# Kernel optimization log

Hardware: AMD Instinct MI355X
Metric: run time of the kernel (lower is better)

Reference implementation:

```python
import jax, jax.numpy as jnp
import numpy as np
from jax import lax

EPS = 1e-5
KV_DOWN = 4

def _bn(z, g, b, m, v):
    # eval-mode BatchNorm2d over channel axis 1
    inv = (g / jnp.sqrt(v + EPS))[None, :, None, None]
    return z * inv + (b - m * g / jnp.sqrt(v + EPS))[None, :, None, None]

def setup_inputs() -> dict:
    key = jax.random.key(0)
    ks = jax.random.split(key, 8)
    B, C, H, W = 8, 256, 128, 128
    AC, VC = 64, 128
    return {
        "x": jax.random.normal(ks[0], (B, C, H, W), jnp.float32),
        "wq": jax.random.normal(ks[1], (AC, C), jnp.float32) * 0.05,
        "wk": jax.random.normal(ks[2], (AC, C), jnp.float32) * 0.05,
        "wv": jax.random.normal(ks[3], (VC, C), jnp.float32) * 0.05,
        "wproj": jax.random.normal(ks[4], (C, VC), jnp.float32) * 0.05,
        "bn_g": jnp.ones((C,), jnp.float32),
        "bn_b": jnp.zeros((C,), jnp.float32),
        "bn_m": jax.random.normal(ks[5], (C,), jnp.float32) * 0.1,
        "bn_v": jax.random.uniform(ks[5], (C,), jnp.float32, 0.5, 1.5),
        "dw_w": jax.random.normal(ks[6], (C, 1, 3, 3), jnp.float32) * 0.1,
        "pw_w": jax.random.normal(ks[7], (C, C), jnp.float32) * 0.05,
        "mbn_g": jnp.ones((C,), jnp.float32),
        "mbn_b": jnp.zeros((C,), jnp.float32),
        "mbn_m": jax.random.normal(ks[7], (C,), jnp.float32) * 0.1,
        "mbn_v": jax.random.uniform(ks[6], (C,), jnp.float32, 0.5, 1.5),
    }

def reference(x, wq, wk, wv, wproj, bn_g, bn_b, bn_m, bn_v, dw_w, pw_w, mbn_g, mbn_b, mbn_m, mbn_v):
    b, c, h, w = x.shape
    d = KV_DOWN
    scale = wq.shape[0] ** -0.5
    # Q from full-res x via 1x1 conv
    q = jnp.einsum('ac,bchw->bahw', wq, x)            # [B,AC,H,W]
    # avg-pool x for K,V
    x_kv = x.reshape(b, c, h // d, d, w // d, d).mean(axis=(3, 5))
    k = jnp.einsum('ac,bchw->bahw', wk, x_kv)          # [B,AC,H',W']
    v = jnp.einsum('vc,bchw->bvhw', wv, x_kv)          # [B,VC,H',W']
    N = h * w
    M = (h // d) * (w // d)
    qf = q.reshape(b, -1, N)                           # [B,AC,N]
    kf = k.reshape(b, -1, M)                           # [B,AC,M]
    vf = v.reshape(b, -1, M)                           # [B,VC,M]
    attn = jnp.einsum('ban,bam->bnm', qf, kf) * scale  # [B,N,M]
    attn = jax.nn.softmax(attn, axis=-1)
    y = jnp.einsum('bnm,bvm->bvn', attn, vf)           # [B,VC,N]
    y = y.reshape(b, vf.shape[1], h, w)
    y = jnp.einsum('cv,bvhw->bchw', wproj, y)          # proj -> [B,C,H,W]
    y = jax.nn.silu(_bn(y, bn_g, bn_b, bn_m, bn_v))
    # depthwise 3x3 + pointwise 1x1 mix
    z = lax.conv_general_dilated(y, dw_w, (1, 1), 'SAME',
                                 dimension_numbers=('NCHW', 'OIHW', 'NCHW'),
                                 feature_group_count=c)
    z = jnp.einsum('oc,bchw->bohw', pw_w, z)
    z = _bn(z, mbn_g, mbn_b, mbn_m, mbn_v)
    return x + jax.nn.silu(z)
```

## Files before the change

### kernel.cpp

```cpp
#include <hip/hip_runtime.h>
#include <hip/hip_bf16.h>
#include <math.h>

#define EPSV 1e-5f

typedef short bf16x8 __attribute__((ext_vector_type(8)));
typedef float f32x16 __attribute__((ext_vector_type(16)));
typedef unsigned int uint4v __attribute__((ext_vector_type(4)));

__device__ __forceinline__ float silu_f(float v) { return v / (1.0f + __expf(-v)); }

__device__ __forceinline__ unsigned short f2bf(float f) {
  __hip_bfloat16 h = __float2bfloat16(f);
  return __builtin_bit_cast(unsigned short, h);
}

__device__ __forceinline__ float fexp2(float x) {
  float r;
  asm("v_exp_f32 %0, %1" : "=v"(r) : "v"(x));
  return r;
}

__device__ __forceinline__ unsigned int cvtpk(float lo, float hi) {
  unsigned int r;
  asm("v_cvt_pk_bf16_f32 %0, %1, %2" : "=v"(r) : "v"(lo), "v"(hi));
  return r;
}

__device__ __forceinline__ bf16x8 ld_frag(const unsigned short* p) {
  return *reinterpret_cast<const bf16x8*>(p);
}

__device__ __forceinline__ void gload16(const unsigned short* g, unsigned short* l) {
  __builtin_amdgcn_global_load_lds((const __attribute__((address_space(1))) void*)g,
                                   (__attribute__((address_space(3))) void*)l, 16, 0, 0);
}

__global__ __launch_bounds__(256) void pool_kernel(const float* __restrict__ x,
                                                   float* __restrict__ xkv) {
  int idx = blockIdx.x * 256 + threadIdx.x;
  int m = idx & 1023, bc = idx >> 10;
  int hh = m >> 5, ww = m & 31;
  const float* base = x + ((size_t)bc << 14) + (size_t)(hh * 4) * 128 + ww * 4;
  float s = 0.f;
#pragma unroll
  for (int i = 0; i < 4; ++i) {
    float4 v = *reinterpret_cast<const float4*>(base + i * 128);
    s += v.x + v.y + v.z + v.w;
  }
  xkv[idx] = s * 0.0625f;
}

__global__ __launch_bounds__(256) void cvtT_kernel(const float* __restrict__ x,
                                                   unsigned short* __restrict__ xbfT) {
  __shared__ unsigned short sT[64 * 68];
  const int tid = threadIdx.x;
  const int b = blockIdx.z, c0 = blockIdx.y * 64, n0 = blockIdx.x * 64;
  const float* xs = x + ((size_t)(b * 256 + c0) << 14) + n0;
#pragma unroll
  for (int pass = 0; pass < 4; ++pass) {
    int cc = (tid >> 4) + pass * 16;
    int col = (tid & 15) * 4;
    float4 v = *reinterpret_cast<const float4*>(xs + ((size_t)cc << 14) + col);
    unsigned short* d = &sT[cc * 68 + col];
    d[0] = f2bf(v.x); d[1] = f2bf(v.y); d[2] = f2bf(v.z); d[3] = f2bf(v.w);
  }
  __syncthreads();
  int n = tid >> 2, cs = (tid & 3) * 16;
  unsigned short tmp[16];
#pragma unroll
  for (int i = 0; i < 16; ++i) tmp[i] = sT[(cs + i) * 68 + n];
  unsigned short* dst = xbfT + (((size_t)b * 16384 + n0 + n) << 8) + c0 + cs;
  *reinterpret_cast<uint4*>(dst) = *reinterpret_cast<uint4*>(tmp);
  *reinterpret_cast<uint4*>(dst + 8) = *reinterpret_cast<uint4*>(tmp + 8);
}

__global__ __launch_bounds__(256) void prep_all(const float* __restrict__ wproj,
                                                const float* __restrict__ bng,
                                                const float* __restrict__ bnb,
                                                const float* __restrict__ bnm,
                                                const float* __restrict__ bnv,
                                                const float* __restrict__ pww,
                                                const float* __restrict__ wq,
                                                unsigned short* __restrict__ wpb,
                                                float* __restrict__ bnsc,
                                                float* __restrict__ bnsh,
                                                unsigned short* __restrict__ pwPack,
                                                unsigned short* __restrict__ wqPack) {
  int i = blockIdx.x * 256 + threadIdx.x;
  if (i < 32768) {
    int j = i & 7, lane = (i >> 3) & 63, kc = (i >> 9) & 7, ctcg = i >> 12;
    int row = (ctcg >> 2) * 128 + (ctcg & 3) * 32 + (lane & 31);
    int col = kc * 16 + (lane >> 5) * 8 + j;
    wpb[i] = f2bf(wproj[row * 128 + col]);
  } else if (i < 33024) {
    int c = i - 32768;
    float inv = bng[c] / sqrtf(bnv[c] + EPSV);
    bnsc[c] = inv;
    bnsh[c] = bnb[c] - bnm[c] * inv;
  } else if (i < 98560) {
    int f = i - 33024;
    int j = f & 7, lane = (f >> 3) & 63, ks = (f >> 9) & 15, mt = f >> 13;
    int o = mt * 32 + (lane & 31);
    int cc = ks * 16 + (lane >> 5) * 8 + j;
    pwPack[f] = f2bf(pww[o * 256 + cc]);
  } else if (i < 114944) {
    int g = i - 98560;
    int j = g & 7, lane = (g >> 3) & 63, ks = (g >> 9) & 15, mt = g >> 13;
    int o = mt * 32 + (lane & 31);
    int cc = ks * 16 + (lane >> 5) * 8 + j;
    wqPack[g] = f2bf(wq[o * 256 + cc] * 0.18033688011112042f);
  }
}

__global__ __launch_bounds__(256, 4) void gemm_kv(const float* __restrict__ wk,
                                                  const float* __restrict__ wv,
                                                  const float* __restrict__ X,
                                                  unsigned short* __restrict__ Kt,
                                                  unsigned short* __restrict__ Vbf) {
  __shared__ float sW[64 * 68];
  __shared__ float sX[64 * 68];
  const int tid = threadIdx.x;
  const int n0 = blockIdx.x * 64;
  const int part = blockIdx.y;
  const int m0 = (part == 0) ? 0 : (part - 1) * 64;
  const float* W = (part == 0) ? wk : wv;
  const size_t xoff = (size_t)blockIdx.z * 256 * 1024;
  const int tm4 = (tid >> 4) * 4, tn4 = (tid & 15) * 4;
  float acc[4][4] = {};
  for (int k0 = 0; k0 < 256; k0 += 64) {
    __syncthreads();
#pragma unroll
    for (int i = 0; i < 16; ++i) {
      int flat = tid + i * 256;
      int kk = flat & 63, mm = flat >> 6;
      sW[kk * 68 + mm] = W[(m0 + mm) * 256 + k0 + kk];
      sX[kk * 68 + mm] = X[xoff + (size_t)(k0 + kk) * 1024 + n0 + mm];
    }
    __syncthreads();
#pragma unroll 8
    for (int k = 0; k < 64; ++k) {
      float4 a4 = *reinterpret_cast<const float4*>(&sW[k * 68 + tm4]);
      float4 b4 = *reinterpret_cast<const float4*>(&sX[k * 68 + tn4]);
      float av[4] = {a4.x, a4.y, a4.z, a4.w};
      float bv[4] = {b4.x, b4.y, b4.z, b4.w};
#pragma unroll
      for (int i = 0; i < 4; ++i)
#pragma unroll
        for (int j = 0; j < 4; ++j) acc[i][j] += av[i] * bv[j];
    }
  }
  if (part == 0) {
    const size_t coff = (size_t)blockIdx.z * 65536;
#pragma unroll
    for (int j = 0; j < 4; ++j) {
      ushort4 o;
      o.x = f2bf(acc[0][j]); o.y = f2bf(acc[1][j]);
      o.z = f2bf(acc[2][j]); o.w = f2bf(acc[3][j]);
      *reinterpret_cast<ushort4*>(&Kt[coff + (size_t)(n0 + tn4 + j) * 64 + tm4]) = o;
    }
  } else {
    const size_t coff = (size_t)blockIdx.z * 131072;
#pragma unroll
    for (int i = 0; i < 4; ++i) {
      ushort4 o;
      o.x = f2bf(acc[i][0]); o.y = f2bf(acc[i][1]);
      o.z = f2bf(acc[i][2]); o.w = f2bf(acc[i][3]);
      *reinterpret_cast<ushort4*>(&Vbf[coff + (size_t)(m0 + tm4 + i) * 1024 + n0 + tn4]) = o;
    }
  }
}

__global__ __launch_bounds__(256, 4) void qgemm_mfma(const unsigned short* __restrict__ xbfT,
                                                     const unsigned short* __restrict__ wqPack,
                                                     unsigned short* __restrict__ Qt) {
  __shared__ __align__(16) unsigned short sX[2][128 * 64];
  const int tid = threadIdx.x;
  const int w = tid >> 6, l = tid & 63;
  const int lq = l & 31, hi = l >> 5;
  const int b = blockIdx.y;
  const int n0 = blockIdx.x * 128;
  const int lr8 = l >> 3;
  const int gslot = (l & 7) ^ (lr8 & 7);
  const unsigned short* xb = xbfT + (((size_t)b * 16384 + n0) << 8);

#define QSTAGE(buf, ck)                                                       \
  {                                                                           \
    _Pragma("unroll") for (int i = 0; i < 4; ++i) {                           \
      int row = w * 32 + i * 8;                                               \
      gload16(xb + ((size_t)(row + lr8) << 8) + (ck) * 64 + gslot * 8,        \
              &sX[buf][row * 64]);                                            \
    }                                                                         \
  }

  f32x16 acc0, acc1;
#pragma unroll
  for (int i = 0; i < 16; ++i) { acc0[i] = 0.f; acc1[i] = 0.f; }

  QSTAGE(0, 0);
  __syncthreads();
  int cur = 0;
  for (int ck = 0; ck < 4; ++ck) {
    if (ck < 3) QSTAGE(cur ^ 1, ck + 1);
    const unsigned short* xl = sX[cur];
#pragma unroll
    for (int k2 = 0; k2 < 4; ++k2) {
      bf16x8 bfr = ld_frag(xl + (w * 32 + lq) * 64 + (((2 * k2 + hi) ^ (lq & 7)) << 3));
      int ks = ck * 4 + k2;
      bf16x8 a0 = ld_frag(wqPack + (size_t)((ks)*64 + l) * 8);
      bf16x8 a1 = ld_frag(wqPack + (size_t)((16 + ks) * 64 + l) * 8);
      acc0 = __builtin_amdgcn_mfma_f32_32x32x16_bf16(a0, bfr, acc0, 0, 0, 0);
      acc1 = __builtin_amdgcn_mfma_f32_32x32x16_bf16(a1, bfr, acc1, 0, 0, 0);
    }
    __syncthreads();
    cur ^= 1;
  }
#undef QSTAGE

  unsigned short* so2 = (unsigned short*)sX + w * 2304;
#pragma unroll
  for (int r = 0; r < 16; ++r) {
    int a = (r & 3) + 8 * (r >> 2) + 4 * hi;
    so2[lq * 72 + a] = f2bf(acc0[r]);
    so2[lq * 72 + 32 + a] = f2bf(acc1[r]);
  }
#pragma unroll
  for (int pass = 0; pass < 4; ++pass) {
    int flat = pass * 64 + l;
    int row = flat >> 3, col8 = (flat & 7) * 8;
    bf16x8 v = ld_frag(so2 + row * 72 + col8);
    *reinterpret_cast<bf16x8*>(Qt + ((size_t)b * 16384 + n0 + w * 32 + row) * 64 + col8) = v;
  }
}

__global__ __launch_bounds__(256, 3) void attn_mfma(
    const unsigned short* __restrict__ Qt, const unsigned short* __restrict__ Kt,
    const unsigned short* __restrict__ Vb, const unsigned short* __restrict__ wpb,
    const float* __restrict__ bnsc, const float* __restrict__ bnsh,
    unsigned short* __restrict__ yact) {
  __shared__ __align__(16) unsigned char smem[49152];
  unsigned short* const sK = (unsigned short*)smem;
  unsigned short* const sV = (unsigned short*)(smem + 16384);
  const int tid = threadIdx.x;
  const int w = tid >> 6, l = tid & 63;
  const int lq = l & 31, hi = l >> 5;
  const int bid = blockIdx.x;
  const int b = bid >> 7;
  const int q0 = (bid & 127) * 128 + w * 32;

  const unsigned short* Qp = Qt + ((size_t)b * 16384 + q0 + lq) * 64 + hi * 8;
  bf16x8 qf[4];
#pragma unroll
  for (int kc = 0; kc < 4; ++kc) qf[kc] = ld_frag(Qp + kc * 16);

  const uint4v ow = {0x3F803F80u, 0x3F803F80u, 0x3F803F80u, 0x3F803F80u};
  const bf16x8 onesf = __builtin_bit_cast(bf16x8, ow);

  f32x16 acc[4], accS;
#pragma unroll
  for (int t = 0; t < 4; ++t)
#pragma unroll
    for (int i = 0; i < 16; ++i) acc[t][i] = 0.f;
#pragma unroll
  for (int i = 0; i < 16; ++i) accS[i] = 0.f;

  const unsigned short* Kb = Kt + (size_t)b * 65536;
  const unsigned short* Vbb = Vb + (size_t)b * 131072;
  const int lr8 = l >> 3;
  const int gslot = (l & 7) ^ (lr8 & 7);

#define STAGE(buf, ch)                                                           \
  {                                                                              \
    const int m0s = (ch) * 64;                                                   \
    _Pragma("unroll") for (int i = 0; i < 2; ++i) {                              \
      int row8 = w * 16 + i * 8;                                                 \
      gload16(Kb + (size_t)(m0s + row8 + lr8) * 64 + gslot * 8,                  \
              sK + (buf) * 4096 + row8 * 64);                                    \
    }                                                                            \
    _Pragma("unroll") for (int j = 0; j < 4; ++j) {                              \
      int vc8 = w * 32 + j * 8;                                                  \
      gload16(Vbb + (size_t)(vc8 + lr8) * 1024 + m0s + gslot * 8,                \
              sV + (buf) * 8192 + vc8 * 64);                                     \
    }                                                                            \
  }

  STAGE(0, 0);
  __syncthreads();
  int cur = 0;
  for (int ch = 0; ch < 16; ++ch) {
    if (ch < 15) STAGE(cur ^ 1, ch + 1);
    const unsigned short* kb = sK + cur * 4096;
    const unsigned short* vb = sV + cur * 8192;
#pragma unroll
    for (int msi = 0; msi < 2; ++msi) {
      const int ms = msi * 32;
      bf16x8 kf[4];
#pragma unroll
      for (int kc = 0; kc < 4; ++kc)
        kf[kc] = ld_frag(kb + (ms + lq) * 64 + (((2 * kc + hi) ^ (lq & 7)) << 3));
      f32x16 sa;
#pragma unroll
      for (int i = 0; i < 16; ++i) sa[i] = 0.f;
      __builtin_amdgcn_s_setprio(1);
#pragma unroll
      for (int kc = 0; kc < 4; ++kc)
        sa = __builtin_amdgcn_mfma_f32_32x32x16_bf16(kf[kc], qf[kc], sa, 0, 0, 0);
      __builtin_amdgcn_s_setprio(0);

      float p[16];
#pragma unroll
      for (int r = 0; r < 16; ++r) p[r] = fexp2(sa[r] - 16.0f);

      unsigned int wpk[8];
#pragma unroll
      for (int i = 0; i < 8; ++i) wpk[i] = cvtpk(p[2 * i], p[2 * i + 1]);
      auto s01 = __builtin_amdgcn_permlane32_swap(wpk[0], wpk[2], false, false);
      auto s23 = __builtin_amdgcn_permlane32_swap(wpk[1], wpk[3], false, false);
      auto s45 = __builtin_amdgcn_permlane32_swap(wpk[4], wpk[6], false, false);
      auto s67 = __builtin_amdgcn_permlane32_swap(wpk[5], wpk[7], false, false);
      uint4v f0 = {(unsigned int)s01[0], (unsigned int)s23[0], (unsigned int)s01[1],
                   (unsigned int)s23[1]};
      uint4v f1 = {(unsigned int)s45[0], (unsigned int)s67[0], (unsigned int)s45[1],
                   (unsigned int)s67[1]};
      bf16x8 pf0 = __builtin_bit_cast(bf16x8, f0);
      bf16x8 pf1 = __builtin_bit_cast(bf16x8, f1);

      __builtin_amdgcn_s_setprio(1);
#pragma unroll
      for (int t = 0; t < 4; ++t) {
        bf16x8 vf0 =
            ld_frag(vb + (t * 32 + lq) * 64 + ((((ms >> 3) + hi) ^ (lq & 7)) << 3));
        bf16x8 vf1 =
            ld_frag(vb + (t * 32 + lq) * 64 + ((((ms >> 3) + 2 + hi) ^ (lq & 7)) << 3));
        acc[t] = __builtin_amdgcn_mfma_f32_32x32x16_bf16(pf0, vf0, acc[t], 0, 0, 0);
        acc[t] = __builtin_amdgcn_mfma_f32_32x32x16_bf16(pf1, vf1, acc[t], 0, 0, 0);
      }
      accS = __builtin_amdgcn_mfma_f32_32x32x16_bf16(pf0, onesf, accS, 0, 0, 0);
      accS = __builtin_amdgcn_mfma_f32_32x32x16_bf16(pf1, onesf, accS, 0, 0, 0);
      __builtin_amdgcn_s_setprio(0);
    }
    __syncthreads();
    cur ^= 1;
  }
#undef STAGE

  unsigned short* so = (unsigned short*)smem + w * 4096;
#pragma unroll
  for (int t = 0; t < 4; ++t)
#pragma unroll
    for (int r = 0; r < 16; ++r) {
      int q = (r & 3) + 8 * (r >> 2) + 4 * hi;
      int col = t * 32 + lq;
      so[q * 128 + (col ^ ((q & 15) << 3))] = f2bf(acc[t][r] / accS[r]);
    }
  __syncthreads();

  bf16x8 of[8];
#pragma unroll
  for (int kc = 0; kc < 8; ++kc) {
    int colr = kc * 16 + hi * 8;
    of[kc] = ld_frag(&so[lq * 128 + (colr ^ ((lq & 15) << 3))]);
  }
#pragma unroll
  for (int cg = 0; cg < 2; ++cg) {
    f32x16 z[4];
#pragma unroll
    for (int t = 0; t < 4; ++t)
#pragma unroll
      for (int i = 0; i < 16; ++i) z[t][i] = 0.f;
#pragma unroll
    for (int ct = 0; ct < 4; ++ct) {
      const unsigned short* wp = wpb + (size_t)(cg * 4 + ct) * 4096 + (size_t)l * 8;
#pragma unroll
      for (int kc = 0; kc < 8; ++kc) {
        bf16x8 wf = ld_frag(wp + kc * 512);
        z[ct] = __builtin_amdgcn_mfma_f32_32x32x16_bf16(wf, of[kc], z[ct], 0, 0, 0);
      }
    }
#pragma unroll
    for (int ct = 0; ct < 4; ++ct)
#pragma unroll
      for (int r = 0; r < 16; ++r) {
        int c = cg * 128 + ct * 32 + (r & 3) + 8 * (r >> 2) + 4 * hi;
        float val = z[ct][r] * bnsc[c] + bnsh[c];
        yact[((size_t)(b * 256 + c)) * 16384 + q0 + lq] = f2bf(silu_f(val));
      }
  }
}

__global__ __launch_bounds__(256, 4) void dwconv_kernel(const unsigned short* __restrict__ yact,
                                                        const float* __restrict__ dww,
                                                        unsigned short* __restrict__ D) {
  __shared__ unsigned int sP[130 * 67];
  const int tid = threadIdx.x;
  const int bc = blockIdx.x;
  const int c = bc & 255;
  for (int s = tid; s < 130 * 67; s += 256) sP[s] = 0;
  __syncthreads();
  const unsigned int* ysrc = reinterpret_cast<const unsigned int*>(yact) + (size_t)bc * 8192;
#pragma unroll
  for (int i = 0; i < 8; ++i) {
    int wi4 = tid + 256 * i;
    uint4 v = *reinterpret_cast<const uint4*>(ysrc + (size_t)wi4 * 4);
    int row = wi4 >> 4;
    int cw = (wi4 & 15) * 4;
    unsigned int* dst = &sP[(row + 1) * 67 + 1 + cw];
    dst[0] = v.x; dst[1] = v.y; dst[2] = v.z; dst[3] = v.w;
  }
  __syncthreads();
  float w9[9];
#pragma unroll
  for (int k = 0; k < 9; ++k) w9[k] = dww[c * 9 + k];
#pragma unroll
  for (int it = 0; it < 4; ++it) {
    int u = tid + 256 * it;
    int rho = u >> 4;
    int wg = u & 15;
    float a0[8] = {}, a1[8] = {};
#pragma unroll
    for (int ir = 0; ir < 4; ++ir) {
      int srow = rho * 2 + ir;
      const unsigned int* rp = &sP[srow * 67 + 4 * wg];
      float f[12];
#pragma unroll
      for (int k = 0; k < 6; ++k) {
        unsigned int wv = rp[k];
        f[2 * k] = __builtin_bit_cast(float, wv << 16);
        f[2 * k + 1] = __builtin_bit_cast(float, wv & 0xffff0000u);
      }
      if (ir < 3) {
#pragma unroll
        for (int cc = 0; cc < 8; ++cc)
#pragma unroll
          for (int dc = 0; dc < 3; ++dc) a0[cc] += f[cc + 1 + dc] * w9[ir * 3 + dc];
      }
      if (ir > 0) {
#pragma unroll
        for (int cc = 0; cc < 8; ++cc)
#pragma unroll
          for (int dc = 0; dc < 3; ++dc) a1[cc] += f[cc + 1 + dc] * w9[(ir - 1) * 3 + dc];
      }
    }
    uint4v o0, o1;
#pragma unroll
    for (int k = 0; k < 4; ++k) {
      o0[k] = (unsigned int)f2bf(a0[2 * k]) | ((unsigned int)f2bf(a0[2 * k + 1]) << 16);
      o1[k] = (unsigned int)f2bf(a1[2 * k]) | ((unsigned int)f2bf(a1[2 * k + 1]) << 16);
    }
    size_t ob = (size_t)bc * 8192 + (size_t)(rho * 2) * 64 + wg * 4;
    unsigned int* Dw = reinterpret_cast<unsigned int*>(D);
    *reinterpret_cast<uint4v*>(Dw + ob) = o0;
    *reinterpret_cast<uint4v*>(Dw + ob + 64) = o1;
  }
}

__global__ __launch_bounds__(256, 2) void pwmix_kernel(
    const unsigned short* __restrict__ D, const unsigned short* __restrict__ pwPack,
    const float* __restrict__ x, const float* __restrict__ mg,
    const float* __restrict__ mb2, const float* __restrict__ mmu,
    const float* __restrict__ mvv, float* __restrict__ out) {
  __shared__ unsigned int sDt[16384];
  __shared__ float smsc[256], smsh[256];
  const int tid = threadIdx.x;
  const int w = tid >> 6, l = tid & 63;
  const int lq = l & 31, hi = l >> 5;
  const int h = blockIdx.x, b = blockIdx.y;
  if (tid < 256) {
    float inv = mg[tid] * rsqrtf(mvv[tid] + EPSV);
    smsc[tid] = inv;
    smsh[tid] = mb2[tid] - mmu[tid] * inv;
  }
  const size_t dbase = ((size_t)b * 256) * 16384 + (size_t)h * 128;
#pragma unroll
  for (int i = 0; i < 8; ++i) {
    int cp = 64 * (i & 1) + 16 * w + (l >> 2);
    int pg = (l & 3) + 4 * (i >> 1);
    const unsigned short* g0 = D + dbase + (size_t)(cp * 2) * 16384 + pg * 8;
    bf16x8 d0 = ld_frag(g0);
    bf16x8 d1 = ld_frag(g0 + 16384);
#pragma unroll
    for (int j = 0; j < 8; ++j) {
      unsigned int word = ((unsigned int)(unsigned short)d0[j]) |
                          (((unsigned int)(unsigned short)d1[j]) << 16);
      int widx = ((pg * 8 + j) * 128 + cp) ^ (j << 2);
      sDt[widx] = word;
    }
  }
  __syncthreads();

  f32x16 z[2][4];
#pragma unroll
  for (int mti = 0; mti < 2; ++mti)
#pragma unroll
    for (int nt = 0; nt < 4; ++nt)
#pragma unroll
      for (int i = 0; i < 16; ++i) z[mti][nt][i] = 0.f;

#pragma unroll
  for (int ks = 0; ks < 16; ++ks) {
    bf16x8 a0 = ld_frag(pwPack + (size_t)(((w * 2 + 0) * 16 + ks) * 64 + l) * 8);
    bf16x8 a1 = ld_frag(pwPack + (size_t)(((w * 2 + 1) * 16 + ks) * 64 + l) * 8);
    bf16x8 bfr[4];
#pragma unroll
    for (int nt = 0; nt < 4; ++nt) {
      int word = ((nt * 32 + lq) * 128 + 8 * ks + 4 * hi) ^ ((lq & 7) << 2);
      bfr[nt] = *reinterpret_cast<const bf16x8*>(
          reinterpret_cast<const unsigned short*>(sDt) + (size_t)word * 2);
    }
#pragma unroll
    for (int nt = 0; nt < 4; ++nt) {
      z[0][nt] = __builtin_amdgcn_mfma_f32_32x32x16_bf16(a0, bfr[nt], z[0][nt], 0, 0, 0);
      z[1][nt] = __builtin_amdgcn_mfma_f32_32x32x16_bf16(a1, bfr[nt], z[1][nt], 0, 0, 0);
    }
  }

#pragma unroll
  for (int mti = 0; mti < 2; ++mti) {
    int ob = (w * 2 + mti) * 32 + 4 * hi;
#pragma unroll
    for (int r = 0; r < 16; ++r) {
      int o = ob + (r & 3) + 8 * (r >> 2);
      float sc = smsc[o], sh = smsh[o];
#pragma unroll
      for (int nt = 0; nt < 4; ++nt) {
        int px = nt * 32 + lq;
        size_t gi = (((size_t)(b * 256 + o)) << 14) + (size_t)h * 128 + px;
        float val = z[mti][nt][r] * sc + sh;
        out[gi] = x[gi] + silu_f(val);
      }
    }
  }
}

extern "C" void kernel_launch(void* const* d_in, const int* in_sizes, int n_in,
                              void* d_out, int out_size, void* d_ws, size_t ws_size,
                              hipStream_t stream) {
  const float* x     = (const float*)d_in[0];
  const float* wq    = (const float*)d_in[1];
  const float* wk    = (const float*)d_in[2];
  const float* wvp   = (const float*)d_in[3];
  const float* wproj = (const float*)d_in[4];
  const float* bng   = (const float*)d_in[5];
  const float* bnb   = (const float*)d_in[6];
  const float* bnm   = (const float*)d_in[7];
  const float* bnv   = (const float*)d_in[8];
  const float* dww   = (const float*)d_in[9];
  const float* pww   = (const float*)d_in[10];
  const float* mg    = (const float*)d_in[11];
  const float* mb2   = (const float*)d_in[12];
  const float* mmu   = (const float*)d_in[13];
  const float* mvv   = (const float*)d_in[14];
  float* out = (float*)d_out;

  char* base = (char*)d_ws;
  unsigned short* D = (unsigned short*)base;
  float* xkv = (float*)base;
  unsigned short* Qt  = (unsigned short*)(base + 8388608);
  unsigned short* Kt  = (unsigned short*)(base + 25165824);
  unsigned short* Vbf = (unsigned short*)(base + 26214400);
  unsigned short* wqPack = (unsigned short*)(base + 28311552);
  float* bnsc = (float*)(base + 67108864);
  float* bnsh = (float*)(base + 67109888);
  unsigned short* wpb    = (unsigned short*)(base + 67110912);
  unsigned short* pwPack = (unsigned short*)(base + 67176448);
  unsigned short* yact   = (unsigned short*)(base + 67307520);
  unsigned short* xbfT   = yact;

  cvtT_kernel<<<dim3(256, 4, 8), 256, 0, stream>>>(x, xbfT);
  pool_kernel<<<8192, 256, 0, stream>>>(x, xkv);
  prep_all<<<449, 256, 0, stream>>>(wproj, bng, bnb, bnm, bnv, pww, wq, wpb, bnsc, bnsh,
                                    pwPack, wqPack);
  gemm_kv<<<dim3(16, 3, 8), 256, 0, stream>>>(wk, wvp, xkv, Kt, Vbf);
  qgemm_mfma<<<dim3(128, 8), 256, 0, stream>>>(xbfT, wqPack, Qt);
  attn_mfma<<<dim3(1024), 256, 0, stream>>>(Qt, Kt, Vbf, wpb, bnsc, bnsh, yact);
  dwconv_kernel<<<2048, 256, 0, stream>>>(yact, dww, D);
  pwmix_kernel<<<dim3(128, 8), 256, 0, stream>>>(D, pwPack, x, mg, mb2, mmu, mvv, out);
}
```

Before: 282.5 us.

## Fuse depthwise 3x3 conv into pointwise mix kernel, dropping intermediate buffer

Merges the depthwise convolution and the pointwise mix into one kernel. Each block handles one image row: it loads a 3-row halo of the activation per 16-channel chunk into LDS, computes the depthwise output on the fly, and writes it as packed bf16 pairs directly into the transposed LDS tile that the MFMA pointwise GEMM consumes. This removes the write and read of the full intermediate D tensor plus one launch. In exchange each activation row is read three times from global memory (cached in L2), with 16 sync-separated chunk iterations and lower per-block parallelism for the depthwise work.

```diff
diff --git a/kernel.cpp b/kernel.cpp
--- a/kernel.cpp
+++ b/kernel.cpp
@@ -25,6 +25,13 @@
   unsigned int r;
   asm("v_cvt_pk_bf16_f32 %0, %1, %2" : "=v"(r) : "v"(lo), "v"(hi));
   return r;
+}
+
+__device__ __forceinline__ float bfu_lo(unsigned int w) {
+  return __builtin_bit_cast(float, w << 16);
+}
+__device__ __forceinline__ float bfu_hi(unsigned int w) {
+  return __builtin_bit_cast(float, w & 0xffff0000u);
 }
 
 __device__ __forceinline__ bf16x8 ld_frag(const unsigned short* p) {
@@ -388,78 +395,14 @@
   }
 }
 
-__global__ __launch_bounds__(256, 4) void dwconv_kernel(const unsigned short* __restrict__ yact,
-                                                        const float* __restrict__ dww,
-                                                        unsigned short* __restrict__ D) {
-  __shared__ unsigned int sP[130 * 67];
-  const int tid = threadIdx.x;
-  const int bc = blockIdx.x;
-  const int c = bc & 255;
-  for (int s = tid; s < 130 * 67; s += 256) sP[s] = 0;
-  __syncthreads();
-  const unsigned int* ysrc = reinterpret_cast<const unsigned int*>(yact) + (size_t)bc * 8192;
-#pragma unroll
-  for (int i = 0; i < 8; ++i) {
-    int wi4 = tid + 256 * i;
-    uint4 v = *reinterpret_cast<const uint4*>(ysrc + (size_t)wi4 * 4);
-    int row = wi4 >> 4;
-    int cw = (wi4 & 15) * 4;
-    unsigned int* dst = &sP[(row + 1) * 67 + 1 + cw];
-    dst[0] = v.x; dst[1] = v.y; dst[2] = v.z; dst[3] = v.w;
-  }
-  __syncthreads();
-  float w9[9];
-#pragma unroll
-  for (int k = 0; k < 9; ++k) w9[k] = dww[c * 9 + k];
-#pragma unroll
-  for (int it = 0; it < 4; ++it) {
-    int u = tid + 256 * it;
-    int rho = u >> 4;
-    int wg = u & 15;
-    float a0[8] = {}, a1[8] = {};
-#pragma unroll
-    for (int ir = 0; ir < 4; ++ir) {
-      int srow = rho * 2 + ir;
-      const unsigned int* rp = &sP[srow * 67 + 4 * wg];
-      float f[12];
-#pragma unroll
-      for (int k = 0; k < 6; ++k) {
-        unsigned int wv = rp[k];
-        f[2 * k] = __builtin_bit_cast(float, wv << 16);
-        f[2 * k + 1] = __builtin_bit_cast(float, wv & 0xffff0000u);
-      }
-      if (ir < 3) {
-#pragma unroll
-        for (int cc = 0; cc < 8; ++cc)
-#pragma unroll
-          for (int dc = 0; dc < 3; ++dc) a0[cc] += f[cc + 1 + dc] * w9[ir * 3 + dc];
-      }
-      if (ir > 0) {
-#pragma unroll
-        for (int cc = 0; cc < 8; ++cc)
-#pragma unroll
-          for (int dc = 0; dc < 3; ++dc) a1[cc] += f[cc + 1 + dc] * w9[(ir - 1) * 3 + dc];
-      }
-    }
-    uint4v o0, o1;
-#pragma unroll
-    for (int k = 0; k < 4; ++k) {
-      o0[k] = (unsigned int)f2bf(a0[2 * k]) | ((unsigned int)f2bf(a0[2 * k + 1]) << 16);
-      o1[k] = (unsigned int)f2bf(a1[2 * k]) | ((unsigned int)f2bf(a1[2 * k + 1]) << 16);
-    }
-    size_t ob = (size_t)bc * 8192 + (size_t)(rho * 2) * 64 + wg * 4;
-    unsigned int* Dw = reinterpret_cast<unsigned int*>(D);
-    *reinterpret_cast<uint4v*>(Dw + ob) = o0;
-    *reinterpret_cast<uint4v*>(Dw + ob + 64) = o1;
-  }
-}
-
-__global__ __launch_bounds__(256, 2) void pwmix_kernel(
-    const unsigned short* __restrict__ D, const unsigned short* __restrict__ pwPack,
-    const float* __restrict__ x, const float* __restrict__ mg,
-    const float* __restrict__ mb2, const float* __restrict__ mmu,
-    const float* __restrict__ mvv, float* __restrict__ out) {
+__global__ __launch_bounds__(256, 2) void dwpw_fused(
+    const unsigned short* __restrict__ yact, const float* __restrict__ dww,
+    const unsigned short* __restrict__ pwPack, const float* __restrict__ x,
+    const float* __restrict__ mg, const float* __restrict__ mb2,
+    const float* __restrict__ mmu, const float* __restrict__ mvv,
+    float* __restrict__ out) {
   __shared__ unsigned int sDt[16384];
+  __shared__ unsigned short sH[16 * 3 * 132];
   __shared__ float smsc[256], smsh[256];
   const int tid = threadIdx.x;
   const int w = tid >> 6, l = tid & 63;
@@ -470,20 +413,53 @@
     smsc[tid] = inv;
     smsh[tid] = mb2[tid] - mmu[tid] * inv;
   }
-  const size_t dbase = ((size_t)b * 256) * 16384 + (size_t)h * 128;
-#pragma unroll
-  for (int i = 0; i < 8; ++i) {
-    int cp = 64 * (i & 1) + 16 * w + (l >> 2);
-    int pg = (l & 3) + 4 * (i >> 1);
-    const unsigned short* g0 = D + dbase + (size_t)(cp * 2) * 16384 + pg * 8;
-    bf16x8 d0 = ld_frag(g0);
-    bf16x8 d1 = ld_frag(g0 + 16384);
-#pragma unroll
-    for (int j = 0; j < 8; ++j) {
-      unsigned int word = ((unsigned int)(unsigned short)d0[j]) |
-                          (((unsigned int)(unsigned short)d1[j]) << 16);
-      int widx = ((pg * 8 + j) * 128 + cp) ^ (j << 2);
-      sDt[widx] = word;
+  for (int s = tid; s < 16 * 3 * 132; s += 256) sH[s] = 0;
+
+  const int cpl = tid >> 5;
+  const int px0 = (tid & 31) * 4;
+
+  for (int chunk = 0; chunk < 16; ++chunk) {
+    __syncthreads();
+    const int c0 = chunk * 16;
+#pragma unroll
+    for (int i = 0; i < 3; ++i) {
+      int u = tid + i * 256;
+      int cc = u / 48, rem = u % 48;
+      int r = rem >> 4, pxg = rem & 15;
+      int hr = h - 1 + r;
+      uint4v vz = {0u, 0u, 0u, 0u};
+      bf16x8 v = __builtin_bit_cast(bf16x8, vz);
+      if (hr >= 0 && hr < 128)
+        v = ld_frag(yact + (size_t)(b * 256 + c0 + cc) * 16384 + hr * 128 + pxg * 8);
+      *reinterpret_cast<bf16x8*>(&sH[(cc * 3 + r) * 132 + 1 + pxg * 8]) = v;
+    }
+    __syncthreads();
+    float d0[4] = {}, d1[4] = {};
+#pragma unroll
+    for (int e = 0; e < 2; ++e) {
+      int cc = cpl * 2 + e;
+      const float* w9 = dww + (c0 + cc) * 9;
+      float wr[9];
+#pragma unroll
+      for (int k = 0; k < 9; ++k) wr[k] = w9[k];
+      float* dd = e ? d1 : d0;
+#pragma unroll
+      for (int r = 0; r < 3; ++r) {
+        const unsigned int* rw =
+            reinterpret_cast<const unsigned int*>(&sH[(cc * 3 + r) * 132 + px0]);
+        unsigned int w0 = rw[0], w1 = rw[1], w2 = rw[2];
+        float fr[6] = {bfu_lo(w0), bfu_hi(w0), bfu_lo(w1),
+                       bfu_hi(w1), bfu_lo(w2), bfu_hi(w2)};
+#pragma unroll
+        for (int p = 0; p < 4; ++p)
+          dd[p] += fr[p] * wr[r * 3] + fr[p + 1] * wr[r * 3 + 1] + fr[p + 2] * wr[r * 3 + 2];
+      }
+    }
+#pragma unroll
+    for (int p = 0; p < 4; ++p) {
+      int px = px0 + p;
+      int widx = (px * 128 + chunk * 8 + cpl) ^ ((px & 7) << 2);
+      sDt[widx] = cvtpk(d0[p], d1[p]);
     }
   }
   __syncthreads();
@@ -553,7 +529,6 @@
   float* out = (float*)d_out;
 
   char* base = (char*)d_ws;
-  unsigned short* D = (unsigned short*)base;
   float* xkv = (float*)base;
   unsigned short* Qt  = (unsigned short*)(base + 8388608);
   unsigned short* Kt  = (unsigned short*)(base + 25165824);
@@ -573,6 +548,6 @@
   gemm_kv<<<dim3(16, 3, 8), 256, 0, stream>>>(wk, wvp, xkv, Kt, Vbf);
   qgemm_mfma<<<dim3(128, 8), 256, 0, stream>>>(xbfT, wqPack, Qt);
   attn_mfma<<<dim3(1024), 256, 0, stream>>>(Qt, Kt, Vbf, wpb, bnsc, bnsh, yact);
-  dwconv_kernel<<<2048, 256, 0, stream>>>(yact, dww, D);
-  pwmix_kernel<<<dim3(128, 8), 256, 0, stream>>>(D, pwPack, x, mg, mb2, mmu, mvv, out);
-}
+  dwpw_fused<<<dim3(128, 8), 256, 0, stream>>>(yact, dww, pwPack, x, mg, mb2, mmu, mvv,
+                                               out);
+}
```

Result: slower. 351.7 us (+24.5%).
